# Kernel optimization log

Hardware: AMD Instinct MI355X
Metric: run time of the kernel (lower is better)

## Reference

```python
import jax, jax.numpy as jnp
import numpy as np


def setup_inputs() -> dict:
    key = jax.random.key(0)
    k1, k2 = jax.random.split(key)
    B, L, D = 32, 1024, 384
    MAX_LEN = 8192
    x = jax.random.normal(k1, (B, L, D), dtype=jnp.float32)
    # float durations in [0, 12); module rounds+clamps internally
    durations = jax.random.uniform(k2, (B, L), dtype=jnp.float32) * 12.0
    return {"x": x, "durations": durations, "max_len": MAX_LEN}


def reference(x, durations, max_len):
    # x: [B, L, D], durations: [B, L] (float), max_len: static python int
    B, L, D = x.shape
    dur = jnp.round(jnp.clip(durations, 0)).astype(jnp.int32)        # [B, L]
    cum = jnp.cumsum(dur, axis=1)                                    # [B, L] exclusive ends
    total = cum[:, -1]                                               # [B] expanded lengths
    t = jnp.arange(max_len, dtype=jnp.int32)                         # [T]
    # frame t belongs to phoneme idx where cum[idx-1] <= t < cum[idx]
    idx = jax.vmap(lambda c: jnp.searchsorted(c, t, side='right'))(cum)  # [B, T]
    idx = jnp.clip(idx, 0, L - 1)
    out = jnp.take_along_axis(x, idx[:, :, None], axis=1)            # [B, T, D]
    mask = (t[None, :] < total[:, None])[:, :, None]                 # [B, T, 1]
    return jnp.where(mask, out, jnp.zeros((), dtype=x.dtype))
```

## Files before the change

### kernel.cpp

```cpp
#include <hip/hip_runtime.h>
#include <hip/hip_bf16.h>


#define B_FIXED 32
#define L_FIXED 1024
#define ROW_F4 96
#define RPB 32

typedef float vfloat4 __attribute__((ext_vector_type(4)));

__global__ __launch_bounds__(1024) void lr_scan_idx_kernel(
    const float* __restrict__ durations, int* __restrict__ idx, int max_len) {
    __shared__ int s[L_FIXED];
    const int b = blockIdx.x;
    const int tid = threadIdx.x;
    float d = durations[b * L_FIXED + tid];
    s[tid] = (int)rintf(fmaxf(d, 0.0f));
    __syncthreads();
    for (int off = 1; off < L_FIXED; off <<= 1) {
        int add = (tid >= off) ? s[tid - off] : 0;
        __syncthreads();
        s[tid] += add;
        __syncthreads();
    }
    const int total = s[L_FIXED - 1];
    for (int t = tid; t < max_len; t += 1024) {
        int lo = 0, hi = L_FIXED;
        while (lo < hi) {
            int mid = (lo + hi) >> 1;
            if (s[mid] <= t) lo = mid + 1; else hi = mid;
        }
        int v = min(lo, L_FIXED - 1);
        idx[b * max_len + t] = (t < total) ? v : -1;
    }
}

__global__ __launch_bounds__(384) void lr_copy_kernel(
    const vfloat4* __restrict__ x, const int* __restrict__ idx,
    vfloat4* __restrict__ out, int max_len) {
    __shared__ int s_idx[RPB];
    const int b = blockIdx.y;
    const int t0 = blockIdx.x * RPB;
    const int lin = threadIdx.y * 96 + threadIdx.x;
    if (lin < RPB) s_idx[lin] = idx[b * max_len + t0 + lin];
    __syncthreads();

    const long xbase = (long)b * L_FIXED * ROW_F4;
    const long obase = ((long)b * max_len + t0) * ROW_F4;
    const int cx = threadIdx.x;
    const int y  = threadIdx.y;
    const vfloat4 zero = {0.f, 0.f, 0.f, 0.f};

#pragma unroll
    for (int k = 0; k < 4; ++k) {
        const int ra = y + 8 * k;
        const int rb = ra + 4;
        const int rowa = s_idx[ra];
        const int rowb = s_idx[rb];
        vfloat4 va = zero, vb = zero;
        if (rowa >= 0) va = x[xbase + (long)rowa * ROW_F4 + cx];
        if (rowb >= 0) vb = x[xbase + (long)rowb * ROW_F4 + cx];
        __builtin_nontemporal_store(va, &out[obase + (long)ra * ROW_F4 + cx]);
        __builtin_nontemporal_store(vb, &out[obase + (long)rb * ROW_F4 + cx]);
    }
}

extern "C" void kernel_launch(void* const* d_in, const int* in_sizes, int n_in,
                              void* d_out, int out_size, void* d_ws, size_t ws_size,
                              hipStream_t stream) {
    const float* x = (const float*)d_in[0];
    const float* durations = (const float*)d_in[1];
    const int MAX_LEN = 8192;

    int* idx = (int*)d_ws;

    lr_scan_idx_kernel<<<B_FIXED, 1024, 0, stream>>>(durations, idx, MAX_LEN);

    dim3 grid(MAX_LEN / RPB, B_FIXED);
    dim3 block(96, 4);
    lr_copy_kernel<<<grid, block, 0, stream>>>(
        (const vfloat4*)x, idx, (vfloat4*)d_out, MAX_LEN);
}
```

Before: 439.3 us.

## Fuse duration scan into copy kernel and enlarge rows per block

```diff
diff --git a/kernel.cpp b/kernel.cpp
--- a/kernel.cpp
+++ b/kernel.cpp
@@ -5,44 +5,44 @@
 #define B_FIXED 32
 #define L_FIXED 1024
 #define ROW_F4 96
-#define RPB 32
+#define RPB 128
 
 typedef float vfloat4 __attribute__((ext_vector_type(4)));
 
-__global__ __launch_bounds__(1024) void lr_scan_idx_kernel(
-    const float* __restrict__ durations, int* __restrict__ idx, int max_len) {
-    __shared__ int s[L_FIXED];
-    const int b = blockIdx.x;
-    const int tid = threadIdx.x;
-    float d = durations[b * L_FIXED + tid];
-    s[tid] = (int)rintf(fmaxf(d, 0.0f));
+__global__ __launch_bounds__(384) void lr_fused_kernel(
+    const float* __restrict__ durations, const vfloat4* __restrict__ x,
+    vfloat4* __restrict__ out, int max_len) {
+    __shared__ int sa[L_FIXED];
+    __shared__ int sb[L_FIXED];
+    __shared__ int s_idx[RPB];
+
+    const int b = blockIdx.y;
+    const int t0 = blockIdx.x * RPB;
+    const int lin = threadIdx.y * 96 + threadIdx.x;
+
+    for (int i = lin; i < L_FIXED; i += 384)
+        sa[i] = (int)rintf(fmaxf(durations[b * L_FIXED + i], 0.0f));
     __syncthreads();
+
+    int* src = sa;
+    int* dst = sb;
     for (int off = 1; off < L_FIXED; off <<= 1) {
-        int add = (tid >= off) ? s[tid - off] : 0;
+        for (int i = lin; i < L_FIXED; i += 384)
+            dst[i] = src[i] + ((i >= off) ? src[i - off] : 0);
         __syncthreads();
-        s[tid] += add;
-        __syncthreads();
+        int* tmp = src; src = dst; dst = tmp;
     }
-    const int total = s[L_FIXED - 1];
-    for (int t = tid; t < max_len; t += 1024) {
+    const int total = src[L_FIXED - 1];
+
+    if (lin < RPB) {
+        const int t = t0 + lin;
         int lo = 0, hi = L_FIXED;
         while (lo < hi) {
             int mid = (lo + hi) >> 1;
-            if (s[mid] <= t) lo = mid + 1; else hi = mid;
+            if (src[mid] <= t) lo = mid + 1; else hi = mid;
         }
-        int v = min(lo, L_FIXED - 1);
-        idx[b * max_len + t] = (t < total) ? v : -1;
+        s_idx[lin] = (t < total) ? min(lo, L_FIXED - 1) : -1;
     }
-}
-
-__global__ __launch_bounds__(384) void lr_copy_kernel(
-    const vfloat4* __restrict__ x, const int* __restrict__ idx,
-    vfloat4* __restrict__ out, int max_len) {
-    __shared__ int s_idx[RPB];
-    const int b = blockIdx.y;
-    const int t0 = blockIdx.x * RPB;
-    const int lin = threadIdx.y * 96 + threadIdx.x;
-    if (lin < RPB) s_idx[lin] = idx[b * max_len + t0 + lin];
     __syncthreads();
 
     const long xbase = (long)b * L_FIXED * ROW_F4;
@@ -52,7 +52,7 @@
     const vfloat4 zero = {0.f, 0.f, 0.f, 0.f};
 
 #pragma unroll
-    for (int k = 0; k < 4; ++k) {
+    for (int k = 0; k < RPB / 8; ++k) {
         const int ra = y + 8 * k;
         const int rb = ra + 4;
         const int rowa = s_idx[ra];
@@ -72,12 +72,8 @@
     const float* durations = (const float*)d_in[1];
     const int MAX_LEN = 8192;
 
-    int* idx = (int*)d_ws;
-
-    lr_scan_idx_kernel<<<B_FIXED, 1024, 0, stream>>>(durations, idx, MAX_LEN);
-
     dim3 grid(MAX_LEN / RPB, B_FIXED);
     dim3 block(96, 4);
-    lr_copy_kernel<<<grid, block, 0, stream>>>(
-        (const vfloat4*)x, idx, (vfloat4*)d_out, MAX_LEN);
+    lr_fused_kernel<<<grid, block, 0, stream>>>(
+        durations, (const vfloat4*)x, (vfloat4*)d_out, MAX_LEN);
 }
```

Result: slower. 462.3 us (+5.2%).

## Remove shared-memory index staging, batch gathers, and swizzle tile order

Applied to the files above, without the earlier changes.

```diff
diff --git a/kernel.cpp b/kernel.cpp
--- a/kernel.cpp
+++ b/kernel.cpp
@@ -38,30 +38,32 @@
 __global__ __launch_bounds__(384) void lr_copy_kernel(
     const vfloat4* __restrict__ x, const int* __restrict__ idx,
     vfloat4* __restrict__ out, int max_len) {
-    __shared__ int s_idx[RPB];
     const int b = blockIdx.y;
-    const int t0 = blockIdx.x * RPB;
-    const int lin = threadIdx.y * 96 + threadIdx.x;
-    if (lin < RPB) s_idx[lin] = idx[b * max_len + t0 + lin];
-    __syncthreads();
+    const int xb = blockIdx.x;
+    const int tile = (xb & 7) * 32 + (xb >> 3);
+    const int t0 = tile * RPB;
 
+    const int cx = threadIdx.x;
+    const int y  = threadIdx.y;
     const long xbase = (long)b * L_FIXED * ROW_F4;
     const long obase = ((long)b * max_len + t0) * ROW_F4;
-    const int cx = threadIdx.x;
-    const int y  = threadIdx.y;
     const vfloat4 zero = {0.f, 0.f, 0.f, 0.f};
+    const int* idx_b = idx + b * max_len + t0 + y;
 
+    int row[8];
 #pragma unroll
-    for (int k = 0; k < 4; ++k) {
-        const int ra = y + 8 * k;
-        const int rb = ra + 4;
-        const int rowa = s_idx[ra];
-        const int rowb = s_idx[rb];
-        vfloat4 va = zero, vb = zero;
-        if (rowa >= 0) va = x[xbase + (long)rowa * ROW_F4 + cx];
-        if (rowb >= 0) vb = x[xbase + (long)rowb * ROW_F4 + cx];
-        __builtin_nontemporal_store(va, &out[obase + (long)ra * ROW_F4 + cx]);
-        __builtin_nontemporal_store(vb, &out[obase + (long)rb * ROW_F4 + cx]);
+    for (int j = 0; j < 8; ++j) row[j] = idx_b[4 * j];
+
+    vfloat4 v[8];
+#pragma unroll
+    for (int j = 0; j < 8; ++j) {
+        v[j] = zero;
+        if (row[j] >= 0) v[j] = x[xbase + (long)row[j] * ROW_F4 + cx];
+    }
+#pragma unroll
+    for (int j = 0; j < 8; ++j) {
+        __builtin_nontemporal_store(
+            v[j], &out[obase + (long)(y + 4 * j) * ROW_F4 + cx]);
     }
 }
 
```

Measured after the change: 559.7 us. +27.4%, slower.
